# Performance work log

Hardware: AMD Instinct MI355X
Metric: run time of the kernel (lower is better)

The kernel has to match this reference:

```python
import jax, jax.numpy as jnp
import numpy as np

S = 8192      # total packed tokens
H = 1152      # hidden size
NH = 16       # heads
HD = 72       # head dim
NSEG = 8      # number of packed (equal-length) sequences
L = S // NSEG # tokens per sequence
SCALE = HD ** -0.5


def setup_inputs() -> dict:
    key = jax.random.key(0)
    ks = jax.random.split(key, 4)
    hidden_states = jax.random.normal(ks[0], (1, S, H), jnp.float32)
    # Real rotary cos/sin per token position within each sequence.
    inv_freq = 1.0 / (10000.0 ** (np.arange(0, HD, 2, dtype=np.float64) / HD))
    freqs = np.outer(np.arange(L, dtype=np.float64), inv_freq)  # [L, HD/2]
    emb = np.concatenate([freqs, freqs], axis=-1)               # [L, HD]
    cos = jnp.asarray(np.tile(np.cos(emb), (NSEG, 1)), jnp.float32)  # [S, HD]
    sin = jnp.asarray(np.tile(np.sin(emb), (NSEG, 1)), jnp.float32)
    Wqkv = jax.random.normal(ks[1], (H, 3 * H), jnp.float32) * (H ** -0.5)
    bqkv = jnp.zeros((3 * H,), jnp.float32)
    Wout = jax.random.normal(ks[2], (H, H), jnp.float32) * (H ** -0.5)
    bout = jnp.zeros((H,), jnp.float32)
    cu_seqlens = jnp.arange(NSEG + 1, dtype=jnp.int32) * L
    return dict(hidden_states=hidden_states, cos=cos, sin=sin,
                Wqkv=Wqkv, bqkv=bqkv, Wout=Wout, bout=bout,
                cu_seqlens=cu_seqlens)


def _rotate_half(x):
    return jnp.concatenate([-x[..., HD // 2:], x[..., :HD // 2]], axis=-1)


def reference(hidden_states, cos, sin, Wqkv, bqkv, Wout, bout, cu_seqlens):
    # QKV projection (fused)
    qkv = hidden_states @ Wqkv + bqkv                 # [1, S, 3H]
    q, k, v = jnp.split(qkv, [H, 2 * H], axis=-1)
    q = q.reshape(1, S, NH, HD)
    k = k.reshape(1, S, NH, HD)
    v = v.reshape(1, S, NH, HD)
    # Inline RoPE on q/k (cos/sin broadcast over heads)
    c = cos[None, :, None, :]
    s = sin[None, :, None, :]
    q = q * c + _rotate_half(q) * s
    k = k * c + _rotate_half(k) * s
    # Varlen (block-diagonal) non-causal attention: equal-length segments
    q = q.reshape(NSEG, L, NH, HD)
    k = k.reshape(NSEG, L, NH, HD)
    v = v.reshape(NSEG, L, NH, HD)
    scores = jnp.einsum('nqhd,nkhd->nhqk', q, k) * SCALE  # [NSEG, NH, L, L]
    probs = jax.nn.softmax(scores, axis=-1)
    ctx = jnp.einsum('nhqk,nkhd->nqhd', probs, v)         # [NSEG, L, NH, HD]
    ctx = ctx.reshape(1, S, H)
    # Output projection
    return ctx @ Wout + bout
```

## Files before the change

kernel.cpp:

```cpp
#include <hip/hip_runtime.h>
#include <hip/hip_fp16.h>
#include <cstdint>

typedef _Float16 half8 __attribute__((ext_vector_type(8)));
typedef _Float16 half4 __attribute__((ext_vector_type(4)));
typedef float floatx4 __attribute__((ext_vector_type(4)));

#define S_TOT 8192
#define H_DIM 1152
#define NHEAD 16
#define HD 72
#define QSTR 96
#define KSTR 104
#define PSTR 76
#define VSTR 76
#define VT_TILE 6080
#define NSEG 8
#define SEGL 1024
#define QSCALE 0.17002324631230988f

__device__ __forceinline__ void gld_lds16(const void* g, void* l) {
  __builtin_amdgcn_global_load_lds((const __attribute__((address_space(1))) void*)g,
                                   (__attribute__((address_space(3))) void*)l, 16, 0, 0);
}

__global__ void cast_f32_f16(const float* __restrict__ in, _Float16* __restrict__ out, int n) {
  int i = (blockIdx.x * 256 + threadIdx.x) * 4;
  if (i < n) {
    float4 v = *(const float4*)(in + i);
    half4 o = { (_Float16)v.x, (_Float16)v.y, (_Float16)v.z, (_Float16)v.w };
    *(half4*)(out + i) = o;
  }
}

__global__ void transpose_cast(const float* __restrict__ W, _Float16* __restrict__ Wt,
                               int R, int C) {
  __shared__ float tile[32][33];
  int tx = threadIdx.x, ty = threadIdx.y;
  int bx = blockIdx.x, by = blockIdx.y;
#pragma unroll
  for (int i = 0; i < 4; ++i)
    tile[ty + i * 8][tx] = W[(size_t)(by * 32 + ty + i * 8) * C + bx * 32 + tx];
  __syncthreads();
#pragma unroll
  for (int i = 0; i < 4; ++i)
    Wt[(size_t)(bx * 32 + ty + i * 8) * R + by * 32 + tx] = (_Float16)tile[tx][ty + i * 8];
}

template <bool OUT_HALF>
__global__ __launch_bounds__(512, 2) void gemm256(
    const _Float16* __restrict__ A, const _Float16* __restrict__ Bt,
    const float* __restrict__ bias, float* __restrict__ Cf, _Float16* __restrict__ Ch,
    int M, int N, int K, int NT, int NWG) {
  extern __shared__ half8 smem8[];
  char* smem = (char*)smem8;
  const int tid = threadIdx.x;
  const int lane = tid & 63;
  const int w = tid >> 6;
  const int quad = lane >> 4, l16 = lane & 15;
  const int wm = w >> 2, wn = w & 3;

  const int orig = blockIdx.x;
  const int wg = (orig & 7) * (NWG >> 3) + (orig >> 3);
  const int mt = wg / NT, nt = wg - mt * NT;
  const int m0 = mt * 256, n0 = nt * 256;

  const _Float16* pA[2];
  const _Float16* pB[2];
  char* ldst[2];
#pragma unroll
  for (int i = 0; i < 2; ++i) {
    int c = i * 512 + tid;
    int r = c >> 2, cs = c & 3;
    int col = ((cs ^ ((r >> 1) & 3)) << 3);
    pA[i] = A + (size_t)(m0 + r) * K + col;
    int br = n0 + r; if (br >= N) br = N - 1;
    pB[i] = Bt + (size_t)br * K + col;
    ldst[i] = smem + c * 16;
  }
  const int e2 = (l16 >> 1) & 3;
  const int rsl = (quad ^ e2) << 4;
  const int aoff = (wm * 128 + l16) * 64 + rsl;
  const int boff = 32768 + (wn * 64 + l16) * 64 + rsl;

  half8 af[4], bf[4];
  floatx4 acc[8][4] = {};

#define STA(s, kh, kcol) { \
  gld_lds16(pA[0] + (kcol) + (kh) * 32, ldst[0] + (s) * 65536 + (kh) * 16384); \
  gld_lds16(pA[1] + (kcol) + (kh) * 32, ldst[1] + (s) * 65536 + (kh) * 16384); }
#define STB(s, kh, kcol) { \
  gld_lds16(pB[0] + (kcol) + (kh) * 32, ldst[0] + (s) * 65536 + 32768 + (kh) * 16384); \
  gld_lds16(pB[1] + (kcol) + (kh) * 32, ldst[1] + (s) * 65536 + 32768 + (kh) * 16384); }
#define LDB4(s, kk) { \
  _Pragma("unroll") for (int in = 0; in < 4; ++in) \
    bf[in] = *(const half8*)(smem + (s) * 65536 + (kk) * 16384 + boff + in * 1024); }
#define LDA4(s, kk, imh) { \
  _Pragma("unroll") for (int j = 0; j < 4; ++j) \
    af[j] = *(const half8*)(smem + (s) * 65536 + (kk) * 16384 + aoff + ((imh) * 4 + j) * 1024); }
#define MFMA16(imh) { \
  __builtin_amdgcn_s_setprio(1); \
  _Pragma("unroll") for (int j = 0; j < 4; ++j) \
  _Pragma("unroll") for (int in = 0; in < 4; ++in) \
    acc[(imh) * 4 + j][in] = \
      __builtin_amdgcn_mfma_f32_16x16x32_f16(af[j], bf[in], acc[(imh) * 4 + j][in], 0, 0, 0); \
  __builtin_amdgcn_s_setprio(0); }
#define BAR() __builtin_amdgcn_s_barrier()
#define LGKM0() { asm volatile("s_waitcnt lgkmcnt(0)" ::: "memory"); __builtin_amdgcn_sched_barrier(0); }
#define VMW(n) asm volatile("s_waitcnt vmcnt(" #n ")" ::: "memory")

  STA(0, 0, 0); STB(0, 0, 0);
  STA(0, 1, 0); STB(0, 1, 0);
  STA(1, 0, 64); STB(1, 0, 64);
  VMW(4);
  BAR();

  const int NI = K >> 7;
#pragma unroll 1
  for (int it = 0; it < NI; ++it) {
    const int kt = it << 7;
    const bool nl = (it + 1 < NI);
    LDB4(0, 0); LDA4(0, 0, 0);
    STA(1, 1, kt + 64);
    BAR(); LGKM0();
    MFMA16(0);
    BAR();
    LDA4(0, 0, 1);
    STB(1, 1, kt + 64);
    BAR(); LGKM0();
    MFMA16(1);
    BAR();
    LDB4(0, 1); LDA4(0, 1, 0);
    if (nl) STA(0, 0, kt + 128);
    BAR(); LGKM0();
    MFMA16(0);
    BAR();
    LDA4(0, 1, 1);
    if (nl) STB(0, 0, kt + 128);
    BAR(); LGKM0();
    MFMA16(1);
    if (nl) { VMW(4); } else { VMW(0); }
    BAR();
    LDB4(1, 0); LDA4(1, 0, 0);
    if (nl) STA(0, 1, kt + 128);
    BAR(); LGKM0();
    MFMA16(0);
    BAR();
    LDA4(1, 0, 1);
    if (nl) STB(0, 1, kt + 128);
    BAR(); LGKM0();
    MFMA16(1);
    BAR();
    LDB4(1, 1); LDA4(1, 1, 0);
    if (nl) STA(1, 0, kt + 192);
    BAR(); LGKM0();
    MFMA16(0);
    BAR();
    LDA4(1, 1, 1);
    if (nl) STB(1, 0, kt + 192);
    BAR(); LGKM0();
    MFMA16(1);
    if (nl) VMW(4);
    BAR();
  }
#undef STA
#undef STB
#undef LDB4
#undef LDA4
#undef MFMA16
#undef BAR
#undef LGKM0
#undef VMW

#pragma unroll
  for (int im = 0; im < 8; ++im) {
    int m = m0 + wm * 128 + im * 16 + quad * 4;
#pragma unroll
    for (int in = 0; in < 4; ++in) {
      int n = n0 + wn * 64 + in * 16 + l16;
      if (n < N) {
        float b = bias[n];
#pragma unroll
        for (int r = 0; r < 4; ++r) {
          float v = acc[im][in][r] + b;
          if (OUT_HALF) Ch[(size_t)(m + r) * N + n] = (_Float16)v;
          else          Cf[(size_t)(m + r) * N + n] = v;
        }
      }
    }
  }
}

__global__ void rope_scatter(const _Float16* __restrict__ QKV,
                             const float* __restrict__ cosb,
                             const float* __restrict__ sinb,
                             _Float16* __restrict__ Qo, _Float16* __restrict__ Ko) {
  int t = blockIdx.x * 256 + threadIdx.x;
  int l = t & 1023, h = (t >> 10) & 15, n = t >> 14;
  int s = n * SEGL + l;
  const _Float16* q = QKV + (size_t)s * 3456 + h * HD;
  const _Float16* k = q + H_DIM;
  const float* cs = cosb + (size_t)s * HD;
  const float* sn = sinb + (size_t)s * HD;
  size_t qo = (size_t)t * QSTR, ko = (size_t)t * KSTR;
  half8 z = {};
  {
    _Float16 qr[72], qv[72];
#pragma unroll
    for (int i = 0; i < 9; ++i) *(half8*)&qr[8 * i] = *(const half8*)(q + 8 * i);
#pragma unroll
    for (int d = 0; d < 36; ++d) {
      float c0 = cs[d], s0 = sn[d], c1 = cs[d + 36], s1 = sn[d + 36];
      float a = (float)qr[d], b = (float)qr[d + 36];
      qv[d]      = (_Float16)((a * c0 - b * s0) * QSCALE);
      qv[d + 36] = (_Float16)((b * c1 + a * s1) * QSCALE);
    }
#pragma unroll
    for (int i = 0; i < 9; ++i) *(half8*)(Qo + qo + 8 * i) = *(half8*)&qv[8 * i];
#pragma unroll
    for (int i = 9; i < 12; ++i) *(half8*)(Qo + qo + 8 * i) = z;
  }
  {
    _Float16 kr[72], kv[72];
#pragma unroll
    for (int i = 0; i < 9; ++i) *(half8*)&kr[8 * i] = *(const half8*)(k + 8 * i);
#pragma unroll
    for (int d = 0; d < 36; ++d) {
      float c0 = cs[d], s0 = sn[d], c1 = cs[d + 36], s1 = sn[d + 36];
      float a = (float)kr[d], b = (float)kr[d + 36];
      kv[d]      = (_Float16)(a * c0 - b * s0);
      kv[d + 36] = (_Float16)(b * c1 + a * s1);
    }
#pragma unroll
    for (int i = 0; i < 9; ++i) *(half8*)(Ko + ko + 8 * i) = *(half8*)&kv[8 * i];
#pragma unroll
    for (int i = 9; i < 13; ++i) *(half8*)(Ko + ko + 8 * i) = z;
  }
}

__global__ __launch_bounds__(256) void transpose_v(const _Float16* __restrict__ QKV,
                                                   _Float16* __restrict__ Vt) {
  __shared__ __align__(16) _Float16 Vs[64 * 88];
  const int tid = threadIdx.x;
  const int kb = blockIdx.x, h = blockIdx.y, n = blockIdx.z;
  const int s0 = n * SEGL + kb * 64;
  const _Float16* src = QKV + (size_t)s0 * 3456 + 2 * H_DIM + h * HD;
  for (int idx = tid; idx < 576; idx += 256) {
    int key = idx / 9, c = idx - key * 9;
    *(half8*)&Vs[key * 88 + c * 8] = *(const half8*)(src + (size_t)key * 3456 + c * 8);
  }
  __syncthreads();
  _Float16* dst = Vt + (((size_t)(n * NHEAD + h)) * 16 + kb) * VT_TILE;
  for (int idx = tid; idx < 800; idx += 256) {
    int d = idx / 10, c = idx - d * 10;
    if (c < 8) {
      half8 v = {};
      if (d < HD) {
#pragma unroll
        for (int j = 0; j < 8; ++j) v[j] = Vs[(c * 8 + j) * 88 + d];
      } else if (d == HD) {
#pragma unroll
        for (int j = 0; j < 8; ++j) v[j] = (_Float16)1.0f;
      }
      *(half8*)(dst + d * VSTR + c * 8) = v;
    } else if (c == 8) {
      *(half8*)(dst + d * VSTR + 64) = half8{};
    } else {
      *(half4*)(dst + d * VSTR + 72) = half4{};
    }
  }
}

__global__ __launch_bounds__(256, 3) void attn_kernel(
    const _Float16* __restrict__ Qb, const _Float16* __restrict__ Kb,
    const _Float16* __restrict__ Vtb, _Float16* __restrict__ Ctx) {
  __shared__ __align__(16) _Float16 Kt[64 * KSTR];
  __shared__ __align__(16) _Float16 Vt[80 * VSTR];
  __shared__ __align__(16) _Float16 Ps[4 * 16 * PSTR];
  const int tid = threadIdx.x;
  const int lane = tid & 63, w = tid >> 6;
  const int quad = lane >> 4, l16 = lane & 15;
  const int id = blockIdx.x;
  const int hn = id & 127, qb = id >> 7;
  const int h = hn >> 3, n = hn & 7;
  const size_t hseg = (size_t)(n * NHEAD + h);
  const _Float16* Qg = Qb + hseg * SEGL * QSTR;
  const _Float16* Kg = Kb + hseg * SEGL * KSTR;
  const _Float16* Vg = Vtb + hseg * 16 * VT_TILE;

  half8 qf[2][3];
#pragma unroll
  for (int qg = 0; qg < 2; ++qg) {
    int row = qb * 128 + w * 32 + qg * 16 + l16;
#pragma unroll
    for (int kc = 0; kc < 3; ++kc)
      qf[qg][kc] = *(const half8*)(Qg + (size_t)row * QSTR + kc * 32 + quad * 8);
  }
  floatx4 o_acc[2][5] = {};

  for (int kb = 0; kb < SEGL / 64; ++kb) {
    __syncthreads();
    {
      const char* base = (const char*)(Kg + (size_t)kb * 64 * KSTR);
#pragma unroll
      for (int i = 0; i < 3; ++i)
        gld_lds16(base + tid * 16 + i * 4096, (char*)Kt + tid * 16 + i * 4096);
      if (tid < 64)
        gld_lds16(base + 12288 + tid * 16, (char*)Kt + 12288 + tid * 16);
    }
    {
      const char* base = (const char*)(Vg + (size_t)kb * VT_TILE);
#pragma unroll
      for (int i = 0; i < 2; ++i)
        gld_lds16(base + tid * 16 + i * 4096, (char*)Vt + tid * 16 + i * 4096);
      if (tid < 248)
        gld_lds16(base + 8192 + tid * 16, (char*)Vt + 8192 + tid * 16);
    }
    __syncthreads();
    floatx4 sa[2][4] = {};
#pragma unroll
    for (int nt = 0; nt < 4; ++nt) {
      half8 kf[3];
#pragma unroll
      for (int kc = 0; kc < 3; ++kc)
        kf[kc] = *(const half8*)&Kt[(nt * 16 + l16) * KSTR + kc * 32 + quad * 8];
#pragma unroll
      for (int qg = 0; qg < 2; ++qg)
#pragma unroll
        for (int kc = 0; kc < 3; ++kc)
          sa[qg][nt] = __builtin_amdgcn_mfma_f32_16x16x32_f16(kf[kc], qf[qg][kc], sa[qg][nt], 0, 0, 0);
    }
#pragma unroll
    for (int qg = 0; qg < 2; ++qg)
#pragma unroll
      for (int nt = 0; nt < 4; ++nt)
#pragma unroll
        for (int r = 0; r < 4; ++r)
          sa[qg][nt][r] = exp2f(sa[qg][nt][r]);
    half8 vf[2][5];
#pragma unroll
    for (int kc2 = 0; kc2 < 2; ++kc2)
#pragma unroll
      for (int t = 0; t < 5; ++t)
        vf[kc2][t] = *(const half8*)&Vt[(t * 16 + l16) * VSTR + kc2 * 32 + quad * 8];
#pragma unroll
    for (int qg = 0; qg < 2; ++qg) {
      int prow = (w * 16 + l16) * PSTR;
#pragma unroll
      for (int nt = 0; nt < 4; ++nt) {
        half4 ph = { (_Float16)sa[qg][nt][0], (_Float16)sa[qg][nt][1],
                     (_Float16)sa[qg][nt][2], (_Float16)sa[qg][nt][3] };
        *(half4*)&Ps[prow + nt * 16 + quad * 4] = ph;
      }
#pragma unroll
      for (int kc2 = 0; kc2 < 2; ++kc2) {
        half8 pb = *(const half8*)&Ps[(w * 16 + l16) * PSTR + kc2 * 32 + quad * 8];
#pragma unroll
        for (int t = 0; t < 5; ++t)
          o_acc[qg][t] = __builtin_amdgcn_mfma_f32_16x16x32_f16(vf[kc2][t], pb, o_acc[qg][t], 0, 0, 0);
      }
    }
  }
#pragma unroll
  for (int qg = 0; qg < 2; ++qg) {
    float lsum = __shfl(o_acc[qg][4][0], 32 + l16, 64);
    float rl = 1.0f / lsum;
    size_t s2 = (size_t)n * SEGL + qb * 128 + w * 32 + qg * 16 + l16;
#pragma unroll
    for (int t = 0; t < 5; ++t) {
      int d0 = t * 16 + quad * 4;
      if (d0 < HD) {
        half4 hv = { (_Float16)(o_acc[qg][t][0] * rl), (_Float16)(o_acc[qg][t][1] * rl),
                     (_Float16)(o_acc[qg][t][2] * rl), (_Float16)(o_acc[qg][t][3] * rl) };
        *(half4*)&Ctx[s2 * H_DIM + h * HD + d0] = hv;
      }
    }
  }
}

extern "C" void kernel_launch(void* const* d_in, const int* in_sizes, int n_in,
                              void* d_out, int out_size, void* d_ws, size_t ws_size,
                              hipStream_t stream) {
  const float* X    = (const float*)d_in[0];
  const float* cosb = (const float*)d_in[1];
  const float* sinb = (const float*)d_in[2];
  const float* Wqkv = (const float*)d_in[3];
  const float* bqkv = (const float*)d_in[4];
  const float* Wout = (const float*)d_in[5];
  const float* bout = (const float*)d_in[6];
  float* out = (float*)d_out;
  char* ws = (char*)d_ws;

  _Float16* Xb   = (_Float16*)(ws);
  _Float16* Wqt  = (_Float16*)(ws + 18874368);
  _Float16* Wot  = (_Float16*)(ws + 26836992);
  _Float16* QKVb = (_Float16*)(ws + 29491200);
  _Float16* Qb   = (_Float16*)(ws + 86114304);
  _Float16* Kb   = (_Float16*)(ws + 111280128);
  _Float16* Vtb  = (_Float16*)(ws + 138543104);
  _Float16* Ctx  = Xb;

  static bool attr_done = false;
  if (!attr_done) {
    hipFuncSetAttribute(reinterpret_cast<const void*>(gemm256<true>),
                        hipFuncAttributeMaxDynamicSharedMemorySize, 131072);
    hipFuncSetAttribute(reinterpret_cast<const void*>(gemm256<false>),
                        hipFuncAttributeMaxDynamicSharedMemorySize, 131072);
    attr_done = true;
  }

  cast_f32_f16<<<9216, 256, 0, stream>>>(X, Xb, S_TOT * H_DIM);
  transpose_cast<<<dim3(108, 36), dim3(32, 8), 0, stream>>>(Wqkv, Wqt, H_DIM, 3 * H_DIM);
  transpose_cast<<<dim3(36, 36), dim3(32, 8), 0, stream>>>(Wout, Wot, H_DIM, H_DIM);
  gemm256<true><<<448, 512, 131072, stream>>>(Xb, Wqt, bqkv, nullptr, QKVb,
                                              S_TOT, 3 * H_DIM, H_DIM, 14, 448);
  rope_scatter<<<512, 256, 0, stream>>>(QKVb, cosb, sinb, Qb, Kb);
  transpose_v<<<dim3(16, 16, 8), 256, 0, stream>>>(QKVb, Vtb);
  attn_kernel<<<1024, 256, 0, stream>>>(Qb, Kb, Vtb, Ctx);
  gemm256<false><<<160, 512, 131072, stream>>>(Ctx, Wot, bout, out, nullptr,
                                               S_TOT, H_DIM, H_DIM, 5, 160);
}
```

Measured before the change: 384.9 us.

## Restructure GEMM mainloop into 4-slot 32-wide K pipeline with XCD-aware tile mapping

The GEMM mainloop now walks K in 32-element steps through a 4-slot ring of 32KB LDS stages, prefetching three steps ahead, instead of 128-wide iterations over two 64KB stages. This is meant to keep more global loads in flight and cut barrier and waitcnt stalls. The workgroup-to-tile mapping also changes: each XCD gets a band of 4 M-tiles and consecutive workgroups walk N, which is meant to improve L2 reuse of A. The new mapping assumes the grid size fits 32 M-tiles times NT, and the loop carries more stage-selection logic that has to be handled carefully.

```diff
diff --git a/kernel.cpp b/kernel.cpp
--- a/kernel.cpp
+++ b/kernel.cpp
@@ -51,7 +51,7 @@
 __global__ __launch_bounds__(512, 2) void gemm256(
     const _Float16* __restrict__ A, const _Float16* __restrict__ Bt,
     const float* __restrict__ bias, float* __restrict__ Cf, _Float16* __restrict__ Ch,
-    int M, int N, int K, int NT, int NWG) {
+    int M, int N, int K, int NT) {
   extern __shared__ half8 smem8[];
   char* smem = (char*)smem8;
   const int tid = threadIdx.x;
@@ -61,13 +61,12 @@
   const int wm = w >> 2, wn = w & 3;
 
   const int orig = blockIdx.x;
-  const int wg = (orig & 7) * (NWG >> 3) + (orig >> 3);
-  const int mt = wg / NT, nt = wg - mt * NT;
+  const int xcd = orig & 7, widx = orig >> 3;
+  const int mt = xcd * 4 + (widx & 3), nt = widx >> 2;
   const int m0 = mt * 256, n0 = nt * 256;
 
   const _Float16* pA[2];
   const _Float16* pB[2];
-  char* ldst[2];
 #pragma unroll
   for (int i = 0; i < 2; ++i) {
     int c = i * 512 + tid;
@@ -76,28 +75,27 @@
     pA[i] = A + (size_t)(m0 + r) * K + col;
     int br = n0 + r; if (br >= N) br = N - 1;
     pB[i] = Bt + (size_t)br * K + col;
-    ldst[i] = smem + c * 16;
-  }
-  const int e2 = (l16 >> 1) & 3;
-  const int rsl = (quad ^ e2) << 4;
+  }
+  const int st0 = tid * 16, st1 = tid * 16 + 8192;
+  const int rsl = ((quad ^ ((l16 >> 1) & 3)) << 4);
   const int aoff = (wm * 128 + l16) * 64 + rsl;
-  const int boff = 32768 + (wn * 64 + l16) * 64 + rsl;
+  const int boff = 16384 + (wn * 64 + l16) * 64 + rsl;
 
   half8 af[4], bf[4];
   floatx4 acc[8][4] = {};
 
-#define STA(s, kh, kcol) { \
-  gld_lds16(pA[0] + (kcol) + (kh) * 32, ldst[0] + (s) * 65536 + (kh) * 16384); \
-  gld_lds16(pA[1] + (kcol) + (kh) * 32, ldst[1] + (s) * 65536 + (kh) * 16384); }
-#define STB(s, kh, kcol) { \
-  gld_lds16(pB[0] + (kcol) + (kh) * 32, ldst[0] + (s) * 65536 + 32768 + (kh) * 16384); \
-  gld_lds16(pB[1] + (kcol) + (kh) * 32, ldst[1] + (s) * 65536 + 32768 + (kh) * 16384); }
-#define LDB4(s, kk) { \
+#define STG_A(ds, kcol) { \
+  gld_lds16(pA[0] + (kcol), smem + (ds) * 32768 + st0); \
+  gld_lds16(pA[1] + (kcol), smem + (ds) * 32768 + st1); }
+#define STG_B(ds, kcol) { \
+  gld_lds16(pB[0] + (kcol), smem + (ds) * 32768 + 16384 + st0); \
+  gld_lds16(pB[1] + (kcol), smem + (ds) * 32768 + 16384 + st1); }
+#define LDB4(s) { \
   _Pragma("unroll") for (int in = 0; in < 4; ++in) \
-    bf[in] = *(const half8*)(smem + (s) * 65536 + (kk) * 16384 + boff + in * 1024); }
-#define LDA4(s, kk, imh) { \
+    bf[in] = *(const half8*)(smem + (s) * 32768 + boff + in * 1024); }
+#define LDA4(s, imh) { \
   _Pragma("unroll") for (int j = 0; j < 4; ++j) \
-    af[j] = *(const half8*)(smem + (s) * 65536 + (kk) * 16384 + aoff + ((imh) * 4 + j) * 1024); }
+    af[j] = *(const half8*)(smem + (s) * 32768 + aoff + ((imh) * 4 + j) * 1024); }
 #define MFMA16(imh) { \
   __builtin_amdgcn_s_setprio(1); \
   _Pragma("unroll") for (int j = 0; j < 4; ++j) \
@@ -107,70 +105,40 @@
   __builtin_amdgcn_s_setprio(0); }
 #define BAR() __builtin_amdgcn_s_barrier()
 #define LGKM0() { asm volatile("s_waitcnt lgkmcnt(0)" ::: "memory"); __builtin_amdgcn_sched_barrier(0); }
-#define VMW(n) asm volatile("s_waitcnt vmcnt(" #n ")" ::: "memory")
-
-  STA(0, 0, 0); STB(0, 0, 0);
-  STA(0, 1, 0); STB(0, 1, 0);
-  STA(1, 0, 64); STB(1, 0, 64);
-  VMW(4);
+
+  STG_A(0, 0);  STG_B(0, 0);
+  STG_A(1, 32); STG_B(1, 32);
+  STG_A(2, 64); STG_B(2, 64);
+  asm volatile("s_waitcnt vmcnt(8)" ::: "memory");
   BAR();
 
-  const int NI = K >> 7;
-#pragma unroll 1
-  for (int it = 0; it < NI; ++it) {
-    const int kt = it << 7;
-    const bool nl = (it + 1 < NI);
-    LDB4(0, 0); LDA4(0, 0, 0);
-    STA(1, 1, kt + 64);
+  const int KT = K >> 5;
+#pragma unroll 4
+  for (int t = 0; t < KT; ++t) {
+    const int slot = t & 3;
+    const int ds = (t + 3) & 3;
+    const bool st = (t + 3) < KT;
+    LDB4(slot); LDA4(slot, 0);
+    if (st) STG_A(ds, (t + 3) * 32);
     BAR(); LGKM0();
     MFMA16(0);
     BAR();
-    LDA4(0, 0, 1);
-    STB(1, 1, kt + 64);
+    LDA4(slot, 1);
+    if (st) STG_B(ds, (t + 3) * 32);
     BAR(); LGKM0();
     MFMA16(1);
+    if (t < KT - 3)       { asm volatile("s_waitcnt vmcnt(8)" ::: "memory"); }
+    else if (t == KT - 3) { asm volatile("s_waitcnt vmcnt(4)" ::: "memory"); }
+    else if (t == KT - 2) { asm volatile("s_waitcnt vmcnt(0)" ::: "memory"); }
     BAR();
-    LDB4(0, 1); LDA4(0, 1, 0);
-    if (nl) STA(0, 0, kt + 128);
-    BAR(); LGKM0();
-    MFMA16(0);
-    BAR();
-    LDA4(0, 1, 1);
-    if (nl) STB(0, 0, kt + 128);
-    BAR(); LGKM0();
-    MFMA16(1);
-    if (nl) { VMW(4); } else { VMW(0); }
-    BAR();
-    LDB4(1, 0); LDA4(1, 0, 0);
-    if (nl) STA(0, 1, kt + 128);
-    BAR(); LGKM0();
-    MFMA16(0);
-    BAR();
-    LDA4(1, 0, 1);
-    if (nl) STB(0, 1, kt + 128);
-    BAR(); LGKM0();
-    MFMA16(1);
-    BAR();
-    LDB4(1, 1); LDA4(1, 1, 0);
-    if (nl) STA(1, 0, kt + 192);
-    BAR(); LGKM0();
-    MFMA16(0);
-    BAR();
-    LDA4(1, 1, 1);
-    if (nl) STB(1, 0, kt + 192);
-    BAR(); LGKM0();
-    MFMA16(1);
-    if (nl) VMW(4);
-    BAR();
-  }
-#undef STA
-#undef STB
+  }
+#undef STG_A
+#undef STG_B
 #undef LDB4
 #undef LDA4
 #undef MFMA16
 #undef BAR
 #undef LGKM0
-#undef VMW
 
 #pragma unroll
   for (int im = 0; im < 8; ++im) {
@@ -413,10 +381,10 @@
   transpose_cast<<<dim3(108, 36), dim3(32, 8), 0, stream>>>(Wqkv, Wqt, H_DIM, 3 * H_DIM);
   transpose_cast<<<dim3(36, 36), dim3(32, 8), 0, stream>>>(Wout, Wot, H_DIM, H_DIM);
   gemm256<true><<<448, 512, 131072, stream>>>(Xb, Wqt, bqkv, nullptr, QKVb,
-                                              S_TOT, 3 * H_DIM, H_DIM, 14, 448);
+                                              S_TOT, 3 * H_DIM, H_DIM, 14);
   rope_scatter<<<512, 256, 0, stream>>>(QKVb, cosb, sinb, Qb, Kb);
   transpose_v<<<dim3(16, 16, 8), 256, 0, stream>>>(QKVb, Vtb);
   attn_kernel<<<1024, 256, 0, stream>>>(Qb, Kb, Vtb, Ctx);
   gemm256<false><<<160, 512, 131072, stream>>>(Ctx, Wot, bout, out, nullptr,
-                                               S_TOT, H_DIM, H_DIM, 5, 160);
-}
+                                               S_TOT, H_DIM, H_DIM, 5);
+}
```

New measurement: 393.2 us. +2.2%, slower.
